# Performance work log

Measured on AMD Instinct MI355X. Metric: run time of the kernel, lower is better.

## Reference

```python
import jax, jax.numpy as jnp
import numpy as np

N = 1 << 20          # number of sample points (rays x samples)
ENC = 32             # hash-grid encoded dim (16 levels x 2 features)
HID = 64
GEO = 15


def setup_inputs() -> dict:
    key = jax.random.key(0)
    ks = jax.random.split(key, 16)
    sc = lambda fan_in: 1.0 / np.sqrt(fan_in)
    return {
        "x": jax.random.normal(ks[0], (N, ENC), jnp.float32),
        "d": jax.random.normal(ks[1], (N, ENC), jnp.float32),
        # sigma net: ENC -> 64 -> 64 -> 1+GEO, bias-free, stored [in, out]
        "Ws0": jax.random.normal(ks[2], (ENC, HID), jnp.float32) * sc(ENC),
        "Ws1": jax.random.normal(ks[3], (HID, HID), jnp.float32) * sc(HID),
        "Ws2": jax.random.normal(ks[4], (HID, 1 + GEO), jnp.float32) * sc(HID),
        # color net: ENC+GEO -> 64 -> 64 -> 64 -> 3, bias-free
        "Wc0": jax.random.normal(ks[5], (ENC + GEO, HID), jnp.float32) * sc(ENC + GEO),
        "Wc1": jax.random.normal(ks[6], (HID, HID), jnp.float32) * sc(HID),
        "Wc2": jax.random.normal(ks[7], (HID, HID), jnp.float32) * sc(HID),
        "Wc3": jax.random.normal(ks[8], (HID, 3), jnp.float32) * sc(HID),
    }


def reference(x, d, Ws0, Ws1, Ws2, Wc0, Wc1, Wc2, Wc3):
    # sigma network: ReLU after EVERY layer (including the last, as in source)
    h = x
    for W in (Ws0, Ws1, Ws2):
        h = jax.nn.relu(h @ W)
    sigma = h[..., 0]            # [N]
    geo_feat = h[..., 1:]        # [N, GEO]

    # color network: ReLU on all but last layer, then sigmoid
    h = jnp.concatenate([d, geo_feat], axis=-1)   # [N, ENC+GEO]
    color_ws = (Wc0, Wc1, Wc2, Wc3)
    for i, W in enumerate(color_ws):
        h = h @ W
        if i != len(color_ws) - 1:
            h = jax.nn.relu(h)
    color = jax.nn.sigmoid(h)    # [N, 3]
    return color, sigma
```

## Files before the change

kernel.cpp:

```cpp
#include <hip/hip_runtime.h>
#include <hip/hip_bf16.h>

typedef short s8v __attribute__((ext_vector_type(8)));
typedef float f4v __attribute__((ext_vector_type(4)));

#define MFMA_BF16 __builtin_amdgcn_mfma_f32_16x16x32_bf16

constexpr int OFF_W0T  = 0;
constexpr int OFF_W1T  = 2560;
constexpr int OFF_W2T  = 7168;
constexpr int OFF_WC0T = 8320;
constexpr int OFF_WC1T = 12928;
constexpr int OFF_WC2T = 17536;
constexpr int OFF_WC3T = 22144;
constexpr int OFF_H    = 23296;
constexpr int SMEM_EL  = 32512;

static __device__ __forceinline__ short bf2s(__hip_bfloat16 h) {
    union { __hip_bfloat16 b; short s; } u; u.b = h; return u.s;
}

__global__ __launch_bounds__(256, 2)
void rf_fused(const void* __restrict__ xv,
              const void* __restrict__ dv,
              const void* __restrict__ Ws0,
              const void* __restrict__ Ws1,
              const void* __restrict__ Ws2,
              const void* __restrict__ Wc0,
              const void* __restrict__ Wc1,
              const void* __restrict__ Wc2,
              const void* __restrict__ Wc3,
              void* __restrict__ outp,
              int npts)
{
    __shared__ __align__(16) short smem[SMEM_EL];
    __shared__ int cls_cnt;
    const int t = threadIdx.x;

    if (t == 0) cls_cnt = 0;
    __syncthreads();
    {
        unsigned short w = ((const unsigned short*)xv)[2 * t];
        int e = (w >> 7) & 0xFF;
        if (e >= 110 && e <= 140) atomicAdd(&cls_cnt, 1);
    }
    __syncthreads();
    const bool isbf = (cls_cnt >= 128);

    auto ldw = [&](const void* p, int idx) -> short {
        if (isbf) return ((const short*)p)[idx];
        return bf2s(__float2bfloat16(((const float*)p)[idx]));
    };

    for (int i = t; i < 2048; i += 256) { int k = i >> 6, n = i & 63; smem[OFF_W0T  + n*40 + k] = ldw(Ws0, i); }
    for (int i = t; i < 4096; i += 256) { int k = i >> 6, n = i & 63; smem[OFF_W1T  + n*72 + k] = ldw(Ws1, i); }
    for (int i = t; i < 1024; i += 256) { int k = i >> 4, n = i & 15; smem[OFF_W2T  + n*72 + k] = ldw(Ws2, i); }
    for (int i = t; i < 4096; i += 256) { int n = i >> 6, k = i & 63; smem[OFF_WC0T + n*72 + k] = (k < 47) ? ldw(Wc0, k*64 + n) : (short)0; }
    for (int i = t; i < 4096; i += 256) { int k = i >> 6, n = i & 63; smem[OFF_WC1T + n*72 + k] = ldw(Wc1, i); }
    for (int i = t; i < 4096; i += 256) { int k = i >> 6, n = i & 63; smem[OFF_WC2T + n*72 + k] = ldw(Wc2, i); }
    for (int i = t; i < 1024; i += 256) { int n = i >> 6, k = i & 63; smem[OFF_WC3T + n*72 + k] = (n < 3) ? ldw(Wc3, k*3 + n) : (short)0; }
    __syncthreads();

    const int lane = t & 63;
    const int wv   = t >> 6;
    const int m16  = lane & 15;
    const int q    = lane >> 4;
    short* sH = smem + OFF_H + wv * 2304;

    const f4v zf = {0.f, 0.f, 0.f, 0.f};

    auto loadRow8 = [&](const void* p, int eoff) -> s8v {
        s8v r;
        if (isbf) {
            r = *(const s8v*)((const short*)p + eoff);
        } else {
            const float* f = (const float*)p + eoff;
            f4v f0 = *(const f4v*)f;
            f4v f1 = *(const f4v*)(f + 4);
            #pragma unroll
            for (int j = 0; j < 4; j++) {
                r[j]     = bf2s(__float2bfloat16(f0[j]));
                r[j + 4] = bf2s(__float2bfloat16(f1[j]));
            }
        }
        return r;
    };
    auto putOut = [&](int idx, float v) {
        if (isbf) ((short*)outp)[idx] = bf2s(__float2bfloat16(v));
        else      ((float*)outp)[idx] = v;
    };

    auto loadAH = [&](s8v (&af)[2][2]) {
        asm volatile("" ::: "memory");
        #pragma unroll
        for (int mt = 0; mt < 2; mt++)
            #pragma unroll
            for (int ks = 0; ks < 2; ks++)
                af[mt][ks] = *(const s8v*)(sH + (mt*16 + m16)*72 + ks*32 + q*8);
    };
    auto layer64 = [&](int woff, f4v (&a)[2][4], const s8v (&af)[2][2]) {
        #pragma unroll
        for (int nt = 0; nt < 4; nt++) {
            s8v b0 = *(const s8v*)(smem + woff + (nt*16 + m16)*72 + q*8);
            s8v b1 = *(const s8v*)(smem + woff + (nt*16 + m16)*72 + 32 + q*8);
            #pragma unroll
            for (int mt = 0; mt < 2; mt++)
                a[mt][nt] = MFMA_BF16(af[mt][1], b1, MFMA_BF16(af[mt][0], b0, zf, 0,0,0), 0,0,0);
        }
    };
    auto storeH64 = [&](const f4v (&a)[2][4]) {
        #pragma unroll
        for (int mt = 0; mt < 2; mt++)
            #pragma unroll
            for (int nt = 0; nt < 4; nt++)
                #pragma unroll
                for (int r = 0; r < 4; r++)
                    sH[(mt*16 + q*4 + r)*72 + nt*16 + m16] =
                        bf2s(__float2bfloat16(fmaxf(a[mt][nt][r], 0.f)));
        asm volatile("" ::: "memory");
    };

    const int ntiles = npts / 32;
    const int nwaves = gridDim.x * 4;
    for (int tile = blockIdx.x*4 + wv; tile < ntiles; tile += nwaves) {
        const int r0 = tile * 32;
        f4v acc[2][4];

        s8v xa[2];
        #pragma unroll
        for (int mt = 0; mt < 2; mt++)
            xa[mt] = loadRow8(xv, (r0 + mt*16 + m16)*32 + q*8);
        #pragma unroll
        for (int nt = 0; nt < 4; nt++) {
            s8v b = *(const s8v*)(smem + OFF_W0T + (nt*16 + m16)*40 + q*8);
            #pragma unroll
            for (int mt = 0; mt < 2; mt++)
                acc[mt][nt] = MFMA_BF16(xa[mt], b, zf, 0,0,0);
        }
        storeH64(acc);

        s8v a2[2][2];
        loadAH(a2);
        layer64(OFF_W1T, acc, a2);
        storeH64(acc);

        s8v a3[2][2];
        loadAH(a3);
        s8v c0 = *(const s8v*)(smem + OFF_W2T + m16*72 + q*8);
        s8v c1 = *(const s8v*)(smem + OFF_W2T + m16*72 + 32 + q*8);
        f4v acc3[2];
        #pragma unroll
        for (int mt = 0; mt < 2; mt++)
            acc3[mt] = MFMA_BF16(a3[mt][1], c1, MFMA_BF16(a3[mt][0], c0, zf, 0,0,0), 0,0,0);

        #pragma unroll
        for (int mt = 0; mt < 2; mt++)
            #pragma unroll
            for (int r = 0; r < 4; r++) {
                float v = fmaxf(acc3[mt][r], 0.f);
                int row = mt*16 + q*4 + r;
                if (m16 == 0) {
                    putOut(3*npts + r0 + row, v);
                    sH[row*72 + 15] = 0;
                } else {
                    sH[row*72 + (m16 - 1)] = bf2s(__float2bfloat16(v));
                }
            }
        asm volatile("" ::: "memory");

        s8v da[2], ga[2];
        #pragma unroll
        for (int mt = 0; mt < 2; mt++) {
            da[mt] = loadRow8(dv, (r0 + mt*16 + m16)*32 + q*8);
            ga[mt] = *(const s8v*)(sH + (mt*16 + m16)*72 + q*8);
        }
        #pragma unroll
        for (int nt = 0; nt < 4; nt++) {
            s8v b0 = *(const s8v*)(smem + OFF_WC0T + (nt*16 + m16)*72 + q*8);
            s8v b1 = *(const s8v*)(smem + OFF_WC0T + (nt*16 + m16)*72 + 32 + q*8);
            #pragma unroll
            for (int mt = 0; mt < 2; mt++)
                acc[mt][nt] = MFMA_BF16(ga[mt], b1, MFMA_BF16(da[mt], b0, zf, 0,0,0), 0,0,0);
        }
        storeH64(acc);

        s8v a5[2][2];
        loadAH(a5);
        layer64(OFF_WC1T, acc, a5);
        storeH64(acc);

        s8v a6[2][2];
        loadAH(a6);
        layer64(OFF_WC2T, acc, a6);
        storeH64(acc);

        s8v a7[2][2];
        loadAH(a7);
        s8v e0 = *(const s8v*)(smem + OFF_WC3T + m16*72 + q*8);
        s8v e1 = *(const s8v*)(smem + OFF_WC3T + m16*72 + 32 + q*8);
        f4v acc7[2];
        #pragma unroll
        for (int mt = 0; mt < 2; mt++)
            acc7[mt] = MFMA_BF16(a7[mt][1], e1, MFMA_BF16(a7[mt][0], e0, zf, 0,0,0), 0,0,0);

        if (m16 < 3) {
            #pragma unroll
            for (int mt = 0; mt < 2; mt++)
                #pragma unroll
                for (int r = 0; r < 4; r++) {
                    float v  = acc7[mt][r];
                    float sg = 1.0f / (1.0f + __expf(-v));
                    putOut((r0 + mt*16 + q*4 + r)*3 + m16, sg);
                }
        }
    }
}

extern "C" void kernel_launch(void* const* d_in, const int* in_sizes, int n_in,
                              void* d_out, int out_size, void* d_ws, size_t ws_size,
                              hipStream_t stream) {
    const int npts = in_sizes[0] / 32;
    rf_fused<<<512, 256, 0, stream>>>(d_in[0], d_in[1], d_in[2], d_in[3], d_in[4],
                                      d_in[5], d_in[6], d_in[7], d_in[8],
                                      d_out, npts);
}
```

Baseline: 351.5 us.

## Double block size, swizzle activation tiles, and prefetch next tile inputs

Blocks grow from 256 to 512 threads (8 waves) with per-wave activation scratch shrunk to a 64-wide XOR-swizzled layout instead of padded stride 72. When inputs are bf16, each wave now loads x and d for its next tile into registers before computing the current one. The d load is also hoisted to the start of the iteration. The goal is to hide global memory latency and keep LDS accesses free of bank conflicts, at the cost of more registers and a launch-bounds change (512,4) that may cause spills.

```diff
diff --git a/kernel.cpp b/kernel.cpp
--- a/kernel.cpp
+++ b/kernel.cpp
@@ -14,13 +14,13 @@
 constexpr int OFF_WC2T = 17536;
 constexpr int OFF_WC3T = 22144;
 constexpr int OFF_H    = 23296;
-constexpr int SMEM_EL  = 32512;
+constexpr int SMEM_EL  = OFF_H + 8 * 2048;
 
 static __device__ __forceinline__ short bf2s(__hip_bfloat16 h) {
     union { __hip_bfloat16 b; short s; } u; u.b = h; return u.s;
 }
 
-__global__ __launch_bounds__(256, 2)
+__global__ __launch_bounds__(512, 4)
 void rf_fused(const void* __restrict__ xv,
               const void* __restrict__ dv,
               const void* __restrict__ Ws0,
@@ -45,43 +45,43 @@
         if (e >= 110 && e <= 140) atomicAdd(&cls_cnt, 1);
     }
     __syncthreads();
-    const bool isbf = (cls_cnt >= 128);
+    const bool isbf = (cls_cnt >= 256);
 
     auto ldw = [&](const void* p, int idx) -> short {
         if (isbf) return ((const short*)p)[idx];
         return bf2s(__float2bfloat16(((const float*)p)[idx]));
     };
 
-    for (int i = t; i < 2048; i += 256) { int k = i >> 6, n = i & 63; smem[OFF_W0T  + n*40 + k] = ldw(Ws0, i); }
-    for (int i = t; i < 4096; i += 256) { int k = i >> 6, n = i & 63; smem[OFF_W1T  + n*72 + k] = ldw(Ws1, i); }
-    for (int i = t; i < 1024; i += 256) { int k = i >> 4, n = i & 15; smem[OFF_W2T  + n*72 + k] = ldw(Ws2, i); }
-    for (int i = t; i < 4096; i += 256) { int n = i >> 6, k = i & 63; smem[OFF_WC0T + n*72 + k] = (k < 47) ? ldw(Wc0, k*64 + n) : (short)0; }
-    for (int i = t; i < 4096; i += 256) { int k = i >> 6, n = i & 63; smem[OFF_WC1T + n*72 + k] = ldw(Wc1, i); }
-    for (int i = t; i < 4096; i += 256) { int k = i >> 6, n = i & 63; smem[OFF_WC2T + n*72 + k] = ldw(Wc2, i); }
-    for (int i = t; i < 1024; i += 256) { int n = i >> 6, k = i & 63; smem[OFF_WC3T + n*72 + k] = (n < 3) ? ldw(Wc3, k*3 + n) : (short)0; }
+    for (int i = t; i < 2048; i += 512) { int k = i >> 6, n = i & 63; smem[OFF_W0T  + n*40 + k] = ldw(Ws0, i); }
+    for (int i = t; i < 4096; i += 512) { int k = i >> 6, n = i & 63; smem[OFF_W1T  + n*72 + k] = ldw(Ws1, i); }
+    for (int i = t; i < 1024; i += 512) { int k = i >> 4, n = i & 15; smem[OFF_W2T  + n*72 + k] = ldw(Ws2, i); }
+    for (int i = t; i < 4096; i += 512) { int n = i >> 6, k = i & 63; smem[OFF_WC0T + n*72 + k] = (k < 47) ? ldw(Wc0, k*64 + n) : (short)0; }
+    for (int i = t; i < 4096; i += 512) { int k = i >> 6, n = i & 63; smem[OFF_WC1T + n*72 + k] = ldw(Wc1, i); }
+    for (int i = t; i < 4096; i += 512) { int k = i >> 6, n = i & 63; smem[OFF_WC2T + n*72 + k] = ldw(Wc2, i); }
+    for (int i = t; i < 1024; i += 512) { int n = i >> 6, k = i & 63; smem[OFF_WC3T + n*72 + k] = (n < 3) ? ldw(Wc3, k*3 + n) : (short)0; }
     __syncthreads();
 
     const int lane = t & 63;
     const int wv   = t >> 6;
     const int m16  = lane & 15;
     const int q    = lane >> 4;
-    short* sH = smem + OFF_H + wv * 2304;
+    short* sH = smem + OFF_H + wv * 2048;
+
+    auto hAddr = [&](int row, int col) -> int {
+        return row*64 + ((((col >> 3) ^ (row & 7))) << 3) + (col & 7);
+    };
 
     const f4v zf = {0.f, 0.f, 0.f, 0.f};
 
-    auto loadRow8 = [&](const void* p, int eoff) -> s8v {
+    auto loadRow8f = [&](const void* p, int eoff) -> s8v {
+        const float* f = (const float*)p + eoff;
+        f4v f0 = *(const f4v*)f;
+        f4v f1 = *(const f4v*)(f + 4);
         s8v r;
-        if (isbf) {
-            r = *(const s8v*)((const short*)p + eoff);
-        } else {
-            const float* f = (const float*)p + eoff;
-            f4v f0 = *(const f4v*)f;
-            f4v f1 = *(const f4v*)(f + 4);
-            #pragma unroll
-            for (int j = 0; j < 4; j++) {
-                r[j]     = bf2s(__float2bfloat16(f0[j]));
-                r[j + 4] = bf2s(__float2bfloat16(f1[j]));
-            }
+        #pragma unroll
+        for (int j = 0; j < 4; j++) {
+            r[j]     = bf2s(__float2bfloat16(f0[j]));
+            r[j + 4] = bf2s(__float2bfloat16(f1[j]));
         }
         return r;
     };
@@ -96,7 +96,7 @@
         for (int mt = 0; mt < 2; mt++)
             #pragma unroll
             for (int ks = 0; ks < 2; ks++)
-                af[mt][ks] = *(const s8v*)(sH + (mt*16 + m16)*72 + ks*32 + q*8);
+                af[mt][ks] = *(const s8v*)(sH + (mt*16 + m16)*64 + (((ks*4 + q) ^ (m16 & 7)) << 3));
     };
     auto layer64 = [&](int woff, f4v (&a)[2][4], const s8v (&af)[2][2]) {
         #pragma unroll
@@ -114,22 +114,57 @@
             #pragma unroll
             for (int nt = 0; nt < 4; nt++)
                 #pragma unroll
-                for (int r = 0; r < 4; r++)
-                    sH[(mt*16 + q*4 + r)*72 + nt*16 + m16] =
+                for (int r = 0; r < 4; r++) {
+                    int row = mt*16 + q*4 + r;
+                    sH[row*64 + (((nt*2 + (m16 >> 3)) ^ (row & 7)) << 3) + (m16 & 7)] =
                         bf2s(__float2bfloat16(fmaxf(a[mt][nt][r], 0.f)));
+                }
         asm volatile("" ::: "memory");
     };
 
     const int ntiles = npts / 32;
-    const int nwaves = gridDim.x * 4;
-    for (int tile = blockIdx.x*4 + wv; tile < ntiles; tile += nwaves) {
-        const int r0 = tile * 32;
+    const int tstep  = gridDim.x * 8;
+    int tile = blockIdx.x * 8 + wv;
+
+    s8v xr[2], dr[2];
+    if (isbf && tile < ntiles) {
+        #pragma unroll
+        for (int mt = 0; mt < 2; mt++) {
+            const int off = (tile*32 + mt*16 + m16)*32 + q*8;
+            xr[mt] = *(const s8v*)((const short*)xv + off);
+            dr[mt] = *(const s8v*)((const short*)dv + off);
+        }
+    }
+
+    for (; tile < ntiles; tile += tstep) {
+        const int r0  = tile * 32;
+        const int nxt = tile + tstep;
+
+        s8v xrn[2], drn[2];
+        if (isbf && nxt < ntiles) {
+            #pragma unroll
+            for (int mt = 0; mt < 2; mt++) {
+                const int off = (nxt*32 + mt*16 + m16)*32 + q*8;
+                xrn[mt] = *(const s8v*)((const short*)xv + off);
+                drn[mt] = *(const s8v*)((const short*)dv + off);
+            }
+        }
+
+        s8v xa[2], da[2];
+        if (isbf) {
+            xa[0] = xr[0]; xa[1] = xr[1];
+            da[0] = dr[0]; da[1] = dr[1];
+        } else {
+            #pragma unroll
+            for (int mt = 0; mt < 2; mt++) {
+                const int off = (r0 + mt*16 + m16)*32 + q*8;
+                xa[mt] = loadRow8f(xv, off);
+                da[mt] = loadRow8f(dv, off);
+            }
+        }
+
         f4v acc[2][4];
 
-        s8v xa[2];
-        #pragma unroll
-        for (int mt = 0; mt < 2; mt++)
-            xa[mt] = loadRow8(xv, (r0 + mt*16 + m16)*32 + q*8);
         #pragma unroll
         for (int nt = 0; nt < 4; nt++) {
             s8v b = *(const s8v*)(smem + OFF_W0T + (nt*16 + m16)*40 + q*8);
@@ -161,19 +196,17 @@
                 int row = mt*16 + q*4 + r;
                 if (m16 == 0) {
                     putOut(3*npts + r0 + row, v);
-                    sH[row*72 + 15] = 0;
+                    sH[hAddr(row, 15)] = 0;
                 } else {
-                    sH[row*72 + (m16 - 1)] = bf2s(__float2bfloat16(v));
+                    sH[hAddr(row, m16 - 1)] = bf2s(__float2bfloat16(v));
                 }
             }
         asm volatile("" ::: "memory");
 
-        s8v da[2], ga[2];
-        #pragma unroll
-        for (int mt = 0; mt < 2; mt++) {
-            da[mt] = loadRow8(dv, (r0 + mt*16 + m16)*32 + q*8);
-            ga[mt] = *(const s8v*)(sH + (mt*16 + m16)*72 + q*8);
-        }
+        s8v ga[2];
+        #pragma unroll
+        for (int mt = 0; mt < 2; mt++)
+            ga[mt] = *(const s8v*)(sH + (mt*16 + m16)*64 + ((q ^ (m16 & 7)) << 3));
         #pragma unroll
         for (int nt = 0; nt < 4; nt++) {
             s8v b0 = *(const s8v*)(smem + OFF_WC0T + (nt*16 + m16)*72 + q*8);
@@ -213,6 +246,11 @@
                     putOut((r0 + mt*16 + q*4 + r)*3 + m16, sg);
                 }
         }
+
+        if (isbf) {
+            xr[0] = xrn[0]; xr[1] = xrn[1];
+            dr[0] = drn[0]; dr[1] = drn[1];
+        }
     }
 }
 
@@ -220,7 +258,7 @@
                               void* d_out, int out_size, void* d_ws, size_t ws_size,
                               hipStream_t stream) {
     const int npts = in_sizes[0] / 32;
-    rf_fused<<<512, 256, 0, stream>>>(d_in[0], d_in[1], d_in[2], d_in[3], d_in[4],
+    rf_fused<<<512, 512, 0, stream>>>(d_in[0], d_in[1], d_in[2], d_in[3], d_in[4],
                                       d_in[5], d_in[6], d_in[7], d_in[8],
                                       d_out, npts);
 }
```

Result: no change. 346.2 us (-1.5%).
